# Performance work log

Hardware: AMD Instinct MI355X
Metric: run time of the kernel (lower is better)

Reference implementation:

```python
import jax, jax.numpy as jnp
import numpy as np

B, C, H, W = 32, 2048, 24, 24
P, RED = 4, 16


def setup_inputs() -> dict:
    key = jax.random.key(0)
    ks = jax.random.split(key, 7)
    return {
        "x": jax.random.normal(ks[0], (B, C, H, W), dtype=jnp.float32),
        "fc1_w": jax.random.normal(ks[1], (C // RED, C), dtype=jnp.float32) * 0.02,
        "fc1_b": jax.random.normal(ks[2], (C // RED,), dtype=jnp.float32) * 0.02,
        "fc2_w": jax.random.normal(ks[3], (C * P, C // RED), dtype=jnp.float32) * 0.02,
        "fc2_b": jax.random.normal(ks[4], (C * P,), dtype=jnp.float32) * 0.02,
        "conv_w": jax.random.normal(ks[5], (C,), dtype=jnp.float32) * 0.02,
        "conv_b": jax.random.normal(ks[6], (C,), dtype=jnp.float32) * 0.02,
    }


def reference(x, fc1_w, fc1_b, fc2_w, fc2_b, conv_w, conv_b):
    # SE-style dynamic weight generation
    pooled = x.mean(axis=(2, 3))                                  # (B, C)
    hidden = jax.nn.silu(pooled @ fc1_w.T + fc1_b)                # (B, C//red)
    dw = (hidden @ fc2_w.T + fc2_b).reshape(B, P, C)              # (B, P, C)
    # depthwise 1x1 conv == per-channel scale + bias
    base = x * conv_w[None, :, None, None] + conv_b[None, :, None, None]
    # per-part channel-weighted reduction: out[b,p,h,w] = sum_c base[b,c,h,w]*dw[b,p,c]
    out = jnp.einsum('bchw,bpc->bphw', base, dw)                  # (B, P, H, W)
    return jax.nn.softmax(out, axis=1)
```

## Files before the change

kernel.cpp:

```cpp
#include <hip/hip_runtime.h>
#include <hip/hip_bf16.h>
#include <math.h>

#define B_ 32
#define C_ 2048
#define HW_ 576
#define P_ 4
#define HID_ 128
#define J_ 8192
#define NCHUNK_ 8
#define NSLOT_ 8

__global__ void pool_trans_kernel(const float* __restrict__ x, float* __restrict__ pooled,
                                  const float* __restrict__ fc2_w, float* __restrict__ wt) {
    int bid = blockIdx.x;
    int tid = threadIdx.x;
    if (bid < 16384) {
        int gwave = bid * 4 + (tid >> 6);
        int lane  = tid & 63;
        const float4* xp4 = (const float4*)(x + (size_t)gwave * HW_);
        float s = 0.f;
        for (int i = lane; i < HW_ / 4; i += 64) {
            float4 v = xp4[i];
            s += v.x + v.y + v.z + v.w;
        }
        #pragma unroll
        for (int off = 32; off > 0; off >>= 1) s += __shfl_down(s, off, 64);
        if (lane == 0) pooled[gwave] = s * (1.0f / (float)HW_);
    } else {
        __shared__ float tile[32][33];
        int bid2 = bid - 16384;
        int kt = bid2 & 3;
        int jt = bid2 >> 2;
        int tx = tid & 31;
        int ty = tid >> 5;
        #pragma unroll
        for (int i = 0; i < 32; i += 8)
            tile[ty + i][tx] = fc2_w[(size_t)(jt * 32 + ty + i) * HID_ + kt * 32 + tx];
        __syncthreads();
        #pragma unroll
        for (int i = 0; i < 32; i += 8)
            wt[(size_t)(kt * 32 + ty + i) * J_ + jt * 32 + tx] = tile[tx][ty + i];
    }
}

__global__ void fc1_kernel(const float* __restrict__ pooled, const float* __restrict__ fc1_w,
                           const float* __restrict__ fc1_b, float* __restrict__ hidden) {
    int o    = blockIdx.x * 4 + (threadIdx.x >> 6);
    int lane = threadIdx.x & 63;
    int b = o >> 7;
    int j = o & 127;
    const float* pr = pooled + (size_t)b * C_;
    const float* wr = fc1_w + (size_t)j * C_;
    float s = 0.f;
    for (int k = lane; k < C_; k += 64) s += pr[k] * wr[k];
    #pragma unroll
    for (int off = 32; off > 0; off >>= 1) s += __shfl_down(s, off, 64);
    if (lane == 0) {
        float z = s + fc1_b[j];
        hidden[o] = z / (1.0f + expf(-z));
    }
}

__global__ void fc2_kernel(const float* __restrict__ hidden, const float* __restrict__ wt,
                           const float* __restrict__ bias, const float* __restrict__ conv_b,
                           float* __restrict__ dw, float* __restrict__ bias_part) {
    int b  = blockIdx.x >> 3;
    int jc = blockIdx.x & 7;
    int tid = threadIdx.x;

    __shared__ float h[HID_];
    if (tid < HID_) h[tid] = hidden[(size_t)b * HID_ + tid];
    __syncthreads();

    int j4 = jc * 256 + tid;
    const float4* wt4 = (const float4*)wt;
    float4 acc = {0.f, 0.f, 0.f, 0.f};
    #pragma unroll 8
    for (int k = 0; k < HID_; ++k) {
        float4 wv = wt4[(size_t)k * (J_ / 4) + j4];
        float hk = h[k];
        acc.x += wv.x * hk;
        acc.y += wv.y * hk;
        acc.z += wv.z * hk;
        acc.w += wv.w * hk;
    }
    const float4* b4 = (const float4*)bias;
    float4 bb = b4[j4];
    acc.x += bb.x; acc.y += bb.y; acc.z += bb.z; acc.w += bb.w;
    ((float4*)(dw + (size_t)b * J_))[j4] = acc;

    int c = (4 * j4) & (C_ - 1);
    float4 cb = *(const float4*)(conv_b + c);
    float local = cb.x * acc.x + cb.y * acc.y + cb.z * acc.z + cb.w * acc.w;
    #pragma unroll
    for (int off = 32; off > 0; off >>= 1) local += __shfl_down(local, off, 64);
    __shared__ float wsum[4];
    if ((tid & 63) == 0) wsum[tid >> 6] = local;
    __syncthreads();
    if (tid == 0) bias_part[(b << 3) + jc] = wsum[0] + wsum[1] + wsum[2] + wsum[3];
}

__global__ void einsum_kernel(const float* __restrict__ x, const float* __restrict__ conv_w,
                              const float* __restrict__ dw, float* __restrict__ part) {
    int b     = blockIdx.x;
    int chunk = blockIdx.y;
    int c0    = chunk * 256;
    int tid   = threadIdx.x;

    __shared__ float4 m4[256];
    __shared__ float4 red[P_ * HW_];
    if (tid < 256) {
        float cw = conv_w[c0 + tid];
        const float* dr = dw + (size_t)b * (P_ * C_) + c0 + tid;
        float4 v;
        v.x = cw * dr[0 * C_];
        v.y = cw * dr[1 * C_];
        v.z = cw * dr[2 * C_];
        v.w = cw * dr[3 * C_];
        m4[tid] = v;
    }
    __syncthreads();

    int g = tid / 144;
    int i = tid - g * 144;

    float4 a0 = {0,0,0,0}, a1 = {0,0,0,0}, a2 = {0,0,0,0}, a3 = {0,0,0,0};
    const float* xb = x + ((size_t)b * C_ + c0) * HW_;
    #pragma unroll 4
    for (int k = 0; k < 64; ++k) {
        int c = g + 4 * k;
        float4 v = ((const float4*)(xb + (size_t)c * HW_))[i];
        float4 m = m4[c];
        a0.x += v.x * m.x; a0.y += v.y * m.x; a0.z += v.z * m.x; a0.w += v.w * m.x;
        a1.x += v.x * m.y; a1.y += v.y * m.y; a1.z += v.z * m.y; a1.w += v.w * m.y;
        a2.x += v.x * m.z; a2.y += v.y * m.z; a2.z += v.z * m.z; a2.w += v.w * m.z;
        a3.x += v.x * m.w; a3.y += v.y * m.w; a3.z += v.z * m.w; a3.w += v.w * m.w;
    }
    red[0 * HW_ + tid] = a0;
    red[1 * HW_ + tid] = a1;
    red[2 * HW_ + tid] = a2;
    red[3 * HW_ + tid] = a3;
    __syncthreads();

    if (g == 0) {
        float4* pp = (float4*)(part + (((size_t)b * NSLOT_ + chunk) * P_) * HW_);
        #pragma unroll
        for (int p = 0; p < P_; ++p) {
            float4 s  = red[p * HW_ + i];
            float4 s1 = red[p * HW_ + 144 + i];
            float4 s2 = red[p * HW_ + 288 + i];
            float4 s3 = red[p * HW_ + 432 + i];
            s.x += s1.x + s2.x + s3.x;
            s.y += s1.y + s2.y + s3.y;
            s.z += s1.z + s2.z + s3.z;
            s.w += s1.w + s2.w + s3.w;
            pp[p * (HW_ / 4) + i] = s;
        }
    }
}

__global__ void softmax_kernel(const float* __restrict__ part, const float* __restrict__ bias_part,
                               float* __restrict__ out) {
    int idx = blockIdx.x * 256 + threadIdx.x;
    int b  = idx / HW_;
    int hw = idx - b * HW_;
    const float* bp = bias_part + b * 8;
    float v0 = bp[0] + bp[1];
    float v1 = bp[2] + bp[3];
    float v2 = bp[4] + bp[5];
    float v3 = bp[6] + bp[7];
    const float* pb = part + ((size_t)b * NSLOT_ * P_) * HW_ + hw;
    #pragma unroll
    for (int s = 0; s < NSLOT_; ++s) {
        const float* ps = pb + (size_t)s * P_ * HW_;
        v0 += ps[0 * HW_];
        v1 += ps[1 * HW_];
        v2 += ps[2 * HW_];
        v3 += ps[3 * HW_];
    }
    float mx = fmaxf(fmaxf(v0, v1), fmaxf(v2, v3));
    float e0 = expf(v0 - mx), e1 = expf(v1 - mx), e2 = expf(v2 - mx), e3 = expf(v3 - mx);
    float inv = 1.0f / (e0 + e1 + e2 + e3);
    float* op = out + ((size_t)b * P_) * HW_ + hw;
    op[0 * HW_] = e0 * inv;
    op[1 * HW_] = e1 * inv;
    op[2 * HW_] = e2 * inv;
    op[3 * HW_] = e3 * inv;
}

extern "C" void kernel_launch(void* const* d_in, const int* in_sizes, int n_in,
                              void* d_out, int out_size, void* d_ws, size_t ws_size,
                              hipStream_t stream) {
    const float* x      = (const float*)d_in[0];
    const float* fc1_w  = (const float*)d_in[1];
    const float* fc1_b  = (const float*)d_in[2];
    const float* fc2_w  = (const float*)d_in[3];
    const float* fc2_b  = (const float*)d_in[4];
    const float* conv_w = (const float*)d_in[5];
    const float* conv_b = (const float*)d_in[6];
    float* out = (float*)d_out;

    float* ws        = (float*)d_ws;
    float* pooled    = ws;
    float* hidden    = pooled + 65536;
    float* dw        = hidden + 4096;
    float* bias_part = dw + 262144;
    float* part      = bias_part + 256;
    float* wt        = part + 589824;

    pool_trans_kernel<<<17408, 256, 0, stream>>>(x, pooled, fc2_w, wt);
    fc1_kernel<<<1024, 256, 0, stream>>>(pooled, fc1_w, fc1_b, hidden);
    fc2_kernel<<<256, 256, 0, stream>>>(hidden, wt, fc2_b, conv_b, dw, bias_part);
    einsum_kernel<<<dim3(B_, NCHUNK_), 576, 0, stream>>>(x, conv_w, dw, part);
    softmax_kernel<<<72, 256, 0, stream>>>(part, bias_part, out);
}
```

Before: 269.1 us.

## Drop fc2 weight transpose, batch fc2 over all samples, split einsum finer

The pass that transposed fc2_w is removed. fc2 now computes 32 output rows for all 32 batch samples per block, so each weight row is read once instead of once per batch, and the output is transposed through shared memory. The conv_b bias reduction moves into the einsum kernel, which now uses 16 channel chunks of 128 (512 blocks) for more parallelism, at the cost of twice the partial sums for softmax to read. Pool and fc1 loads are vectorized and unrolled.

```diff
diff --git a/kernel.cpp b/kernel.cpp
--- a/kernel.cpp
+++ b/kernel.cpp
@@ -1,5 +1,4 @@
 #include <hip/hip_runtime.h>
-#include <hip/hip_bf16.h>
 #include <math.h>
 
 #define B_ 32
@@ -8,40 +7,22 @@
 #define P_ 4
 #define HID_ 128
 #define J_ 8192
-#define NCHUNK_ 8
-#define NSLOT_ 8
-
-__global__ void pool_trans_kernel(const float* __restrict__ x, float* __restrict__ pooled,
-                                  const float* __restrict__ fc2_w, float* __restrict__ wt) {
-    int bid = blockIdx.x;
-    int tid = threadIdx.x;
-    if (bid < 16384) {
-        int gwave = bid * 4 + (tid >> 6);
-        int lane  = tid & 63;
-        const float4* xp4 = (const float4*)(x + (size_t)gwave * HW_);
-        float s = 0.f;
-        for (int i = lane; i < HW_ / 4; i += 64) {
-            float4 v = xp4[i];
-            s += v.x + v.y + v.z + v.w;
-        }
-        #pragma unroll
-        for (int off = 32; off > 0; off >>= 1) s += __shfl_down(s, off, 64);
-        if (lane == 0) pooled[gwave] = s * (1.0f / (float)HW_);
-    } else {
-        __shared__ float tile[32][33];
-        int bid2 = bid - 16384;
-        int kt = bid2 & 3;
-        int jt = bid2 >> 2;
-        int tx = tid & 31;
-        int ty = tid >> 5;
-        #pragma unroll
-        for (int i = 0; i < 32; i += 8)
-            tile[ty + i][tx] = fc2_w[(size_t)(jt * 32 + ty + i) * HID_ + kt * 32 + tx];
-        __syncthreads();
-        #pragma unroll
-        for (int i = 0; i < 32; i += 8)
-            wt[(size_t)(kt * 32 + ty + i) * J_ + jt * 32 + tx] = tile[tx][ty + i];
-    }
+#define NCHUNK_ 16
+#define CSZ_ 128
+
+__global__ void pool_kernel(const float* __restrict__ x, float* __restrict__ pooled) {
+    int gwave = blockIdx.x * 4 + (threadIdx.x >> 6);
+    int lane  = threadIdx.x & 63;
+    const float* xr = x + (size_t)gwave * HW_;
+    const float4* xp4 = (const float4*)xr;
+    float4 v0 = xp4[lane];
+    float4 v1 = xp4[lane + 64];
+    float s = v0.x + v0.y + v0.z + v0.w
+            + v1.x + v1.y + v1.z + v1.w
+            + xr[512 + lane];
+    #pragma unroll
+    for (int off = 32; off > 0; off >>= 1) s += __shfl_down(s, off, 64);
+    if (lane == 0) pooled[gwave] = s * (1.0f / (float)HW_);
 }
 
 __global__ void fc1_kernel(const float* __restrict__ pooled, const float* __restrict__ fc1_w,
@@ -50,10 +31,15 @@
     int lane = threadIdx.x & 63;
     int b = o >> 7;
     int j = o & 127;
-    const float* pr = pooled + (size_t)b * C_;
-    const float* wr = fc1_w + (size_t)j * C_;
+    const float4* pr = (const float4*)(pooled + (size_t)b * C_);
+    const float4* wr = (const float4*)(fc1_w + (size_t)j * C_);
     float s = 0.f;
-    for (int k = lane; k < C_; k += 64) s += pr[k] * wr[k];
+    #pragma unroll
+    for (int i = 0; i < 8; ++i) {
+        float4 p = pr[lane + 64 * i];
+        float4 w = wr[lane + 64 * i];
+        s += p.x * w.x + p.y * w.y + p.z * w.z + p.w * w.w;
+    }
     #pragma unroll
     for (int off = 32; off > 0; off >>= 1) s += __shfl_down(s, off, 64);
     if (lane == 0) {
@@ -62,65 +48,88 @@
     }
 }
 
-__global__ void fc2_kernel(const float* __restrict__ hidden, const float* __restrict__ wt,
-                           const float* __restrict__ bias, const float* __restrict__ conv_b,
-                           float* __restrict__ dw, float* __restrict__ bias_part) {
-    int b  = blockIdx.x >> 3;
-    int jc = blockIdx.x & 7;
+__global__ void fc2_kernel(const float* __restrict__ hidden, const float* __restrict__ fc2_w,
+                           const float* __restrict__ fc2_b, float* __restrict__ dw) {
+    __shared__ float h[32][132];
+    __shared__ float dt[32][33];
     int tid = threadIdx.x;
-
-    __shared__ float h[HID_];
-    if (tid < HID_) h[tid] = hidden[(size_t)b * HID_ + tid];
-    __syncthreads();
-
-    int j4 = jc * 256 + tid;
-    const float4* wt4 = (const float4*)wt;
-    float4 acc = {0.f, 0.f, 0.f, 0.f};
+    int jbase = blockIdx.x * 32;
+
+    {
+        int bb = tid >> 3, q = tid & 7;
+        const float4* hb = (const float4*)(hidden + (size_t)bb * HID_);
+        #pragma unroll
+        for (int m = 0; m < 4; ++m) {
+            float4 v = hb[q + 8 * m];
+            int k = (q + 8 * m) * 4;
+            h[bb][k] = v.x; h[bb][k + 1] = v.y; h[bb][k + 2] = v.z; h[bb][k + 3] = v.w;
+        }
+    }
+    __syncthreads();
+
+    int b  = tid & 31;
+    int jl = tid >> 5;
+    int j0 = jbase + jl * 4;
+    const float4* W = (const float4*)(fc2_w + (size_t)j0 * HID_);
+    float a0 = fc2_b[j0], a1 = fc2_b[j0 + 1], a2 = fc2_b[j0 + 2], a3 = fc2_b[j0 + 3];
     #pragma unroll 8
-    for (int k = 0; k < HID_; ++k) {
-        float4 wv = wt4[(size_t)k * (J_ / 4) + j4];
-        float hk = h[k];
-        acc.x += wv.x * hk;
-        acc.y += wv.y * hk;
-        acc.z += wv.z * hk;
-        acc.w += wv.w * hk;
-    }
-    const float4* b4 = (const float4*)bias;
-    float4 bb = b4[j4];
-    acc.x += bb.x; acc.y += bb.y; acc.z += bb.z; acc.w += bb.w;
-    ((float4*)(dw + (size_t)b * J_))[j4] = acc;
-
-    int c = (4 * j4) & (C_ - 1);
-    float4 cb = *(const float4*)(conv_b + c);
-    float local = cb.x * acc.x + cb.y * acc.y + cb.z * acc.z + cb.w * acc.w;
-    #pragma unroll
-    for (int off = 32; off > 0; off >>= 1) local += __shfl_down(local, off, 64);
-    __shared__ float wsum[4];
-    if ((tid & 63) == 0) wsum[tid >> 6] = local;
-    __syncthreads();
-    if (tid == 0) bias_part[(b << 3) + jc] = wsum[0] + wsum[1] + wsum[2] + wsum[3];
+    for (int k4 = 0; k4 < 32; ++k4) {
+        float4 hv = *(const float4*)(&h[b][k4 * 4]);
+        float4 wa = W[k4], wb = W[32 + k4], wc = W[64 + k4], wd = W[96 + k4];
+        a0 += hv.x * wa.x + hv.y * wa.y + hv.z * wa.z + hv.w * wa.w;
+        a1 += hv.x * wb.x + hv.y * wb.y + hv.z * wb.z + hv.w * wb.w;
+        a2 += hv.x * wc.x + hv.y * wc.y + hv.z * wc.z + hv.w * wc.w;
+        a3 += hv.x * wd.x + hv.y * wd.y + hv.z * wd.z + hv.w * wd.w;
+    }
+    dt[jl * 4 + 0][b] = a0;
+    dt[jl * 4 + 1][b] = a1;
+    dt[jl * 4 + 2][b] = a2;
+    dt[jl * 4 + 3][b] = a3;
+    __syncthreads();
+
+    int b2 = tid >> 3, q2 = tid & 7;
+    float4 o;
+    o.x = dt[q2 * 4 + 0][b2];
+    o.y = dt[q2 * 4 + 1][b2];
+    o.z = dt[q2 * 4 + 2][b2];
+    o.w = dt[q2 * 4 + 3][b2];
+    ((float4*)(dw + (size_t)b2 * J_ + jbase))[q2] = o;
 }
 
 __global__ void einsum_kernel(const float* __restrict__ x, const float* __restrict__ conv_w,
-                              const float* __restrict__ dw, float* __restrict__ part) {
+                              const float* __restrict__ conv_b, const float* __restrict__ dw,
+                              float* __restrict__ part, float* __restrict__ bias_part) {
     int b     = blockIdx.x;
     int chunk = blockIdx.y;
-    int c0    = chunk * 256;
+    int c0    = chunk * CSZ_;
     int tid   = threadIdx.x;
 
-    __shared__ float4 m4[256];
+    __shared__ float4 m4[CSZ_];
     __shared__ float4 red[P_ * HW_];
-    if (tid < 256) {
-        float cw = conv_w[c0 + tid];
-        const float* dr = dw + (size_t)b * (P_ * C_) + c0 + tid;
-        float4 v;
-        v.x = cw * dr[0 * C_];
-        v.y = cw * dr[1 * C_];
-        v.z = cw * dr[2 * C_];
-        v.w = cw * dr[3 * C_];
-        m4[tid] = v;
-    }
-    __syncthreads();
+    __shared__ float4 bsum[2];
+    if (tid < CSZ_) {
+        int c = c0 + tid;
+        float cw = conv_w[c], cb = conv_b[c];
+        const float* dr = dw + (size_t)b * J_ + c;
+        float d0 = dr[0 * C_], d1 = dr[1 * C_], d2 = dr[2 * C_], d3 = dr[3 * C_];
+        float4 mv; mv.x = cw * d0; mv.y = cw * d1; mv.z = cw * d2; mv.w = cw * d3;
+        m4[tid] = mv;
+        float4 bp; bp.x = cb * d0; bp.y = cb * d1; bp.z = cb * d2; bp.w = cb * d3;
+        #pragma unroll
+        for (int off = 32; off > 0; off >>= 1) {
+            bp.x += __shfl_down(bp.x, off, 64);
+            bp.y += __shfl_down(bp.y, off, 64);
+            bp.z += __shfl_down(bp.z, off, 64);
+            bp.w += __shfl_down(bp.w, off, 64);
+        }
+        if ((tid & 63) == 0) bsum[tid >> 6] = bp;
+    }
+    __syncthreads();
+    if (tid == 0) {
+        float4 t0 = bsum[0], t1 = bsum[1];
+        float4 r; r.x = t0.x + t1.x; r.y = t0.y + t1.y; r.z = t0.z + t1.z; r.w = t0.w + t1.w;
+        *(float4*)(bias_part + ((size_t)(b * NCHUNK_ + chunk)) * 4) = r;
+    }
 
     int g = tid / 144;
     int i = tid - g * 144;
@@ -128,7 +137,7 @@
     float4 a0 = {0,0,0,0}, a1 = {0,0,0,0}, a2 = {0,0,0,0}, a3 = {0,0,0,0};
     const float* xb = x + ((size_t)b * C_ + c0) * HW_;
     #pragma unroll 4
-    for (int k = 0; k < 64; ++k) {
+    for (int k = 0; k < CSZ_ / 4; ++k) {
         int c = g + 4 * k;
         float4 v = ((const float4*)(xb + (size_t)c * HW_))[i];
         float4 m = m4[c];
@@ -144,7 +153,7 @@
     __syncthreads();
 
     if (g == 0) {
-        float4* pp = (float4*)(part + (((size_t)b * NSLOT_ + chunk) * P_) * HW_);
+        float4* pp = (float4*)(part + ((size_t)(b * NCHUNK_ + chunk) * P_) * HW_);
         #pragma unroll
         for (int p = 0; p < P_; ++p) {
             float4 s  = red[p * HW_ + i];
@@ -165,14 +174,16 @@
     int idx = blockIdx.x * 256 + threadIdx.x;
     int b  = idx / HW_;
     int hw = idx - b * HW_;
-    const float* bp = bias_part + b * 8;
-    float v0 = bp[0] + bp[1];
-    float v1 = bp[2] + bp[3];
-    float v2 = bp[4] + bp[5];
-    float v3 = bp[6] + bp[7];
-    const float* pb = part + ((size_t)b * NSLOT_ * P_) * HW_ + hw;
-    #pragma unroll
-    for (int s = 0; s < NSLOT_; ++s) {
+    const float4* bp = (const float4*)(bias_part + (size_t)b * NCHUNK_ * 4);
+    float v0 = 0.f, v1 = 0.f, v2 = 0.f, v3 = 0.f;
+    #pragma unroll
+    for (int s = 0; s < NCHUNK_; ++s) {
+        float4 t = bp[s];
+        v0 += t.x; v1 += t.y; v2 += t.z; v3 += t.w;
+    }
+    const float* pb = part + ((size_t)b * NCHUNK_ * P_) * HW_ + hw;
+    #pragma unroll
+    for (int s = 0; s < NCHUNK_; ++s) {
         const float* ps = pb + (size_t)s * P_ * HW_;
         v0 += ps[0 * HW_];
         v1 += ps[1 * HW_];
@@ -206,12 +217,11 @@
     float* hidden    = pooled + 65536;
     float* dw        = hidden + 4096;
     float* bias_part = dw + 262144;
-    float* part      = bias_part + 256;
-    float* wt        = part + 589824;
-
-    pool_trans_kernel<<<17408, 256, 0, stream>>>(x, pooled, fc2_w, wt);
+    float* part      = bias_part + 2048;
+
+    pool_kernel<<<16384, 256, 0, stream>>>(x, pooled);
     fc1_kernel<<<1024, 256, 0, stream>>>(pooled, fc1_w, fc1_b, hidden);
-    fc2_kernel<<<256, 256, 0, stream>>>(hidden, wt, fc2_b, conv_b, dw, bias_part);
-    einsum_kernel<<<dim3(B_, NCHUNK_), 576, 0, stream>>>(x, conv_w, dw, part);
+    fc2_kernel<<<256, 256, 0, stream>>>(hidden, fc2_w, fc2_b, dw);
+    einsum_kernel<<<dim3(B_, NCHUNK_), 576, 0, stream>>>(x, conv_w, conv_b, dw, part, bias_part);
     softmax_kernel<<<72, 256, 0, stream>>>(part, bias_part, out);
 }
```

New measurement: 257.3 us. -4.4%, faster.
